# Performance work log

Measured on AMD Instinct MI355X. Metric: run time of the kernel, lower is better.

Reference implementation:

```python
import jax, jax.numpy as jnp
import numpy as np

TOP_P = 0.9
NEG_FILL = -100000.0
POS_FILL = 100000.0


def setup_inputs() -> dict:
    key = jax.random.key(0)
    k1, k2, k3 = jax.random.split(key, 3)
    B, S, V = 256, 128, 128000
    input_ids = jax.random.randint(k1, (B, S), 0, V, dtype=jnp.int64)
    logits = jax.random.normal(k2, (B, V), dtype=jnp.float32)
    # uniform watermark keys xi in (0,1); avoid exact 0 for log
    xi = jax.random.uniform(k3, (V,), dtype=jnp.float32, minval=1e-6, maxval=1.0)
    return {"input_ids": input_ids, "logits": logits, "xi": xi}


def reference(input_ids, logits, xi):
    B, V = logits.shape
    probs = jax.nn.softmax(logits, axis=-1)                       # [B, V]
    order = jnp.argsort(-probs, axis=-1)                          # descending sort indices [B, V]
    sorted_probs = jnp.take_along_axis(probs, order, axis=-1)     # [B, V]
    cum = jnp.cumsum(sorted_probs, axis=-1)                       # [B, V]
    # torch.searchsorted(cum, top_p, right=False) == count of cum < top_p
    cutoff = jnp.sum(cum < TOP_P, axis=-1)                        # [B]
    keep = jnp.arange(V)[None, :] <= cutoff[:, None]              # keep [:cutoff+1]
    # exponential-minimum trick: argmin over -log(xi)/p within the top-p set
    scores = -jnp.log(xi[order]) / sorted_probs                   # [B, V]
    scores = jnp.where(keep, scores, jnp.inf)
    pos = jnp.argmin(scores, axis=-1)                             # [B]
    next_token = jnp.take_along_axis(order, pos[:, None], axis=-1)[:, 0]  # [B]
    out = jnp.full_like(logits, NEG_FILL)
    out = out.at[jnp.arange(B), next_token].set(POS_FILL)
    return out
```

## Files before the change

kernel.cpp:

```cpp
#include <hip/hip_runtime.h>
#include <hip/hip_bf16.h>
#include <math.h>


constexpr int   NBINS     = 4096;
constexpr float BIN_MIN   = -8.0f;
constexpr float BIN_SCALE = 256.0f;
constexpr float BIN_OFF   = 2048.0f;
constexpr float BIN_W     = 1.0f / 256.0f;
constexpr int   STASH_CAP = 4096;
constexpr int   BINB_CAP  = 512;
constexpr int   WIN       = 6;
constexpr int   MAXC      = 96;
constexpr float CAND_THR  = -3.0f;
constexpr float NEG_FILL  = -100000.0f;
constexpr float POS_FILL  =  100000.0f;
constexpr float TOPP      = 0.9f;
constexpr int   BPR_FILL  = 32;

struct Ws {
    float*    key;
    unsigned* candIdx;
    float*    candKey;
    int*      candCnt;
    unsigned long long* winner;
};

__device__ __forceinline__ unsigned sortable(float f) {
    unsigned u = __float_as_uint(f);
    return (u & 0x80000000u) ? ~u : (u | 0x80000000u);
}
__device__ __forceinline__ int binOf(float l) {
    int b = (int)fmaf(l, BIN_SCALE, BIN_OFF);
    return min(max(b, 0), NBINS - 1);
}

__global__ __launch_bounds__(256)
void k0_keys(const float4* __restrict__ xi4, float* __restrict__ key,
             unsigned* __restrict__ candIdx, float* __restrict__ candKey,
             int* __restrict__ candCnt, int V4)
{
    __shared__ int cnt;
    __shared__ unsigned sIdx[MAXC];
    __shared__ float    sKey[MAXC];
    if (threadIdx.x == 0) cnt = 0;
    __syncthreads();

    const int f = blockIdx.x * 256 + threadIdx.x;
    if (f < V4) {
        float4 x = xi4[f];
        float kv[4];
        kv[0] = __logf(-__logf(x.x));
        kv[1] = __logf(-__logf(x.y));
        kv[2] = __logf(-__logf(x.z));
        kv[3] = __logf(-__logf(x.w));
        reinterpret_cast<float4*>(key)[f] = make_float4(kv[0], kv[1], kv[2], kv[3]);
        #pragma unroll
        for (int c = 0; c < 4; ++c) {
            if (kv[c] < CAND_THR) {
                int p = atomicAdd(&cnt, 1);
                if (p < MAXC) { sIdx[p] = (unsigned)(f * 4 + c); sKey[p] = kv[c]; }
            }
        }
    }
    __syncthreads();
    const int base = blockIdx.x * MAXC;
    const int n = min(cnt, MAXC);
    for (int i = threadIdx.x; i < MAXC; i += 256) {
        candIdx[base + i] = (i < n) ? sIdx[i] : 0u;
        candKey[base + i] = (i < n) ? sKey[i] : INFINITY;
    }
    if (threadIdx.x == 0) candCnt[blockIdx.x] = cnt;
}

__device__ __forceinline__ void scan_bins(const unsigned* lh, int lane,
                                          int& candBin, double& candS, double& target)
{
    const int hi = NBINS - 1 - (lane << 6);
    double seg = 0.0;
    for (int k = 0; k < 64; ++k) {
        int b = hi - k;
        seg += (double)lh[b] * (double)__expf(fmaf((float)b + 0.5f, BIN_W, BIN_MIN));
    }
    double v = seg;
    for (int off = 1; off < 64; off <<= 1) {
        double u = __shfl_up(v, off);
        if (lane >= off) v += u;
    }
    double excl = v - seg;
    double total = __shfl(v, 63);
    target = TOPP * total;

    candBin = -1; candS = 0.0;
    double cum = excl;
    for (int k = 0; k < 64; ++k) {
        int b = hi - k;
        double h = (double)lh[b] * (double)__expf(fmaf((float)b + 0.5f, BIN_W, BIN_MIN));
        if (candBin < 0 && cum + h >= target) { candBin = b; candS = cum; }
        cum += h;
    }
    for (int off = 32; off >= 1; off >>= 1) {
        int    ob = __shfl_xor(candBin, off);
        double os = __shfl_xor(candS, off);
        if (ob > candBin) { candBin = ob; candS = os; }
    }
}

__global__ __launch_bounds__(1024)
void kb_row(const float* __restrict__ logits, const float* __restrict__ key,
            const unsigned* __restrict__ candIdx, const float* __restrict__ candKey,
            const int* __restrict__ candCnt, unsigned long long* __restrict__ winner,
            int V, int nchunk, int nslots)
{
    const int row = blockIdx.x;
    const int tid = threadIdx.x;
    const int n4  = V >> 2;
    const float* rowp = logits + (size_t)row * V;
    const float4* p4 = reinterpret_cast<const float4*>(rowp);

    __shared__ unsigned lh[NBINS];
    __shared__ float  s_sl[STASH_CAP];
    __shared__ int    s_si[STASH_CAP];
    __shared__ float  s_bl[BINB_CAP];
    __shared__ int    s_bi[BINB_CAP];
    __shared__ double s_be[BINB_CAP];
    __shared__ unsigned long long wrd[16];
    __shared__ float  wrf[16];
    __shared__ int   sStashCnt, sB2, sBtil, sB, sM, sNeedFull, sCandOver;
    __shared__ float sLmax, sLcut;
    __shared__ int   sIcut;
    __shared__ double sCumAbove, sTarget;
    __shared__ unsigned long long sBest;

    for (int i = tid; i < NBINS; i += 1024) lh[i] = 0u;
    if (tid == 0) { sStashCnt = 0; sB2 = 0; sCandOver = 0; sNeedFull = 0; }
    __syncthreads();
    if (tid < nchunk && candCnt[tid] > MAXC) atomicOr(&sCandOver, 1);

    for (int k = 0; k < 8; ++k) {
        int j = tid + k * 4000;
        float4 L = p4[j];
        atomicAdd(&lh[binOf(L.x)], 1u);
        atomicAdd(&lh[binOf(L.y)], 1u);
        atomicAdd(&lh[binOf(L.z)], 1u);
        atomicAdd(&lh[binOf(L.w)], 1u);
    }
    __syncthreads();
    if (tid < 64) {
        int b; double cs, tg;
        scan_bins(lh, tid, b, cs, tg);
        if (tid == 0) sBtil = b;
    }
    __syncthreads();
    const int wlo = max(0, sBtil - WIN);
    const int whi = min(NBINS - 1, sBtil + WIN);

    for (int i = tid; i < NBINS; i += 1024) lh[i] = 0u;
    __syncthreads();

    float lmax = -INFINITY;
    for (int j = tid; j < n4; j += 1024) {
        float4 L = p4[j];
        float lv[4] = {L.x, L.y, L.z, L.w};
        #pragma unroll
        for (int c = 0; c < 4; ++c) {
            float l = lv[c];
            int b = binOf(l);
            atomicAdd(&lh[b], 1u);
            lmax = fmaxf(lmax, l);
            if ((unsigned)(b - wlo) <= (unsigned)(whi - wlo)) {
                int p = atomicAdd(&sStashCnt, 1);
                if (p < STASH_CAP) { s_sl[p] = l; s_si[p] = j * 4 + c; }
            }
        }
    }
    for (int off = 32; off >= 1; off >>= 1)
        lmax = fmaxf(lmax, __shfl_down(lmax, off));
    if ((tid & 63) == 0) wrf[tid >> 6] = lmax;
    __syncthreads();
    if (tid == 0) {
        float m = wrf[0];
        for (int w = 1; w < 16; ++w) m = fmaxf(m, wrf[w]);
        sLmax = m;
    }
    __syncthreads();

    if (tid < 64) {
        int b; double cs, tg;
        scan_bins(lh, tid, b, cs, tg);
        if (tid == 0) { sB = b; sCumAbove = cs; sTarget = tg; }
    }
    __syncthreads();
    const int B = sB;

    const bool stashOK = (B >= wlo) && (B <= whi) && (sStashCnt <= STASH_CAP);
    if (stashOK) {
        const int n = sStashCnt;
        for (int i = tid; i < n; i += 1024) {
            float l = s_sl[i];
            if (binOf(l) == B) {
                int q = atomicAdd(&sB2, 1);
                if (q < BINB_CAP) { s_bl[q] = l; s_bi[q] = s_si[i]; }
            }
        }
    } else {
        for (int j = tid; j < n4; j += 1024) {
            float4 L = p4[j];
            float lv[4] = {L.x, L.y, L.z, L.w};
            #pragma unroll
            for (int c = 0; c < 4; ++c) {
                if (binOf(lv[c]) == B) {
                    int q = atomicAdd(&sB2, 1);
                    if (q < BINB_CAP) { s_bl[q] = lv[c]; s_bi[q] = j * 4 + c; }
                }
            }
        }
    }
    __syncthreads();
    int nB = min(sB2, BINB_CAP);
    if (sB2 > BINB_CAP && tid == 0) sNeedFull = 1;

    int P = 1; while (P < nB) P <<= 1;
    if (P < 2) P = 2;
    for (int i = tid; i < P; i += 1024)
        if (i >= nB) { s_bl[i] = -INFINITY; s_bi[i] = 0x7fffffff; }
    for (int size = 2; size <= P; size <<= 1) {
        for (int stride = size >> 1; stride > 0; stride >>= 1) {
            __syncthreads();
            if (tid < P) {
                int i = tid, jj = tid ^ stride;
                if (jj > i) {
                    float li = s_bl[i], lj = s_bl[jj];
                    int   ii = s_bi[i], ij = s_bi[jj];
                    bool up = ((i & size) == 0);
                    bool iBeforeJ = (li > lj) || (li == lj && ii < ij);
                    bool sw = up ? (!iBeforeJ && !(li == lj && ii == ij)) : iBeforeJ;
                    if (sw) {
                        s_bl[i] = lj; s_bl[jj] = li;
                        s_bi[i] = ij; s_bi[jj] = ii;
                    }
                }
            }
        }
    }
    __syncthreads();

    for (int i = tid; i < nB; i += 1024) s_be[i] = exp((double)s_bl[i]);
    __syncthreads();
    if (tid == 0) {
        double cum = sCumAbove, target = sTarget;
        int m = nB;
        for (int k = 0; k < nB; ++k) {
            cum += s_be[k];
            if (cum >= target) { m = k + 1; break; }
        }
        m = max(m, 1);
        sM = m;
        sLcut = s_bl[m - 1];
        sIcut = s_bi[m - 1];
    }
    __syncthreads();
    const float lcut = sLcut;
    const int   icut = sIcut;

    unsigned long long best = ~0ull;
    for (int s = tid; s < nslots; s += 1024) {
        unsigned idx = candIdx[s];
        float ck = candKey[s];
        float l = rowp[idx];
        bool kept = (l > lcut) || (l == lcut && (int)idx <= icut);
        if (kept) {
            unsigned long long pack =
                ((unsigned long long)sortable(ck - l) << 32) | idx;
            best = pack < best ? pack : best;
        }
    }
    for (int off = 32; off >= 1; off >>= 1) {
        unsigned long long o = __shfl_down(best, off);
        best = o < best ? o : best;
    }
    if ((tid & 63) == 0) wrd[tid >> 6] = best;
    __syncthreads();
    if (tid == 0) {
        unsigned long long b = wrd[0];
        for (int w = 1; w < 16; ++w) b = wrd[w] < b ? wrd[w] : b;
        sBest = b;
        unsigned bound = sortable(CAND_THR - sLmax);
        if (!((unsigned)(b >> 32) < bound) || sCandOver) sNeedFull = 1;
    }
    __syncthreads();

    if (sNeedFull) {
        for (int j = tid; j < V; j += 1024) {
            float l = rowp[j];
            bool kept = (l > lcut) || (l == lcut && j <= icut);
            if (kept) {
                unsigned long long pack =
                    ((unsigned long long)sortable(key[j] - l) << 32) | (unsigned)j;
                best = pack < best ? pack : best;
            }
        }
        for (int off = 32; off >= 1; off >>= 1) {
            unsigned long long o = __shfl_down(best, off);
            best = o < best ? o : best;
        }
        if ((tid & 63) == 0) wrd[tid >> 6] = best;
        __syncthreads();
        if (tid == 0) {
            unsigned long long b = sBest;
            for (int w = 0; w < 16; ++w) b = wrd[w] < b ? wrd[w] : b;
            sBest = b;
        }
        __syncthreads();
    }

    if (tid == 0) winner[row] = sBest;
}

__global__ __launch_bounds__(256)
void kd_fill(float* __restrict__ out,
             const unsigned long long* __restrict__ winner, int V)
{
    const int row = blockIdx.x / BPR_FILL;
    const int seg = blockIdx.x % BPR_FILL;
    const int n4  = V >> 2;
    const int per = n4 / BPR_FILL;
    const int start = seg * per;
    const int end = (seg == BPR_FILL - 1) ? n4 : start + per;
    float4* o4 = reinterpret_cast<float4*>(out + (size_t)row * V);

    const unsigned win = (unsigned)(winner[row] & 0xffffffffu);
    const int winj = (int)(win >> 2);

    const float4 nf = make_float4(NEG_FILL, NEG_FILL, NEG_FILL, NEG_FILL);
    for (int j = start + threadIdx.x; j < end; j += 256) {
        float4 v = nf;
        if (j == winj) {
            float ov[4] = {v.x, v.y, v.z, v.w};
            ov[win & 3] = POS_FILL;
            v = make_float4(ov[0], ov[1], ov[2], ov[3]);
        }
        o4[j] = v;
    }
}

extern "C" void kernel_launch(void* const* d_in, const int* in_sizes, int n_in,
                              void* d_out, int out_size, void* d_ws, size_t ws_size,
                              hipStream_t stream) {
    const float* logits = (const float*)d_in[1];
    const float* xi     = (const float*)d_in[2];
    float*       out    = (float*)d_out;
    const int V = in_sizes[2];
    const int B = in_sizes[1] / V;
    const int V4 = V / 4;
    const int nchunk = (V + 1023) / 1024;
    const int nslots = nchunk * MAXC;

    char* w = (char*)d_ws;
    size_t off = 0;
    Ws ws;
    ws.key     = (float*)(w + off);    off += (size_t)V * sizeof(float);
    off = (off + 255) & ~(size_t)255;
    ws.candIdx = (unsigned*)(w + off); off += (size_t)nslots * sizeof(unsigned);
    ws.candKey = (float*)(w + off);    off += (size_t)nslots * sizeof(float);
    ws.candCnt = (int*)(w + off);      off += (size_t)nchunk * sizeof(int);
    off = (off + 255) & ~(size_t)255;
    ws.winner  = (unsigned long long*)(w + off); off += (size_t)B * sizeof(unsigned long long);

    k0_keys<<<(V4 + 255) / 256, 256, 0, stream>>>((const float4*)xi, ws.key,
                                                  ws.candIdx, ws.candKey, ws.candCnt, V4);
    kb_row <<<B, 1024, 0, stream>>>(logits, ws.key, ws.candIdx, ws.candKey,
                                    ws.candCnt, ws.winner, V, nchunk, nslots);
    kd_fill<<<B * BPR_FILL, 256, 0, stream>>>(out, ws.winner, V);
}
```

Before: 291.2 us.

## Split per-row histogram sweep across slice blocks and simplify bin resolution

The single per-row block that built the histogram and stash is split into a separate kernel where 8 blocks per row each histogram one slice and record a slice max, writing partial histograms to workspace. A resolve kernel sums the partials, rescans the full row for the boundary bin, and ranks bin members with an O(n^2) rank sort instead of a bitonic sort. This raises parallelism for the memory-bound sweep (256 blocks to 2048) but adds partial-histogram global traffic, an extra launch, and a second full row read in the resolve kernel since the stash is removed.

```diff
diff --git a/kernel.cpp b/kernel.cpp
--- a/kernel.cpp
+++ b/kernel.cpp
@@ -8,21 +8,22 @@
 constexpr float BIN_SCALE = 256.0f;
 constexpr float BIN_OFF   = 2048.0f;
 constexpr float BIN_W     = 1.0f / 256.0f;
-constexpr int   STASH_CAP = 4096;
 constexpr int   BINB_CAP  = 512;
-constexpr int   WIN       = 6;
 constexpr int   MAXC      = 96;
 constexpr float CAND_THR  = -3.0f;
 constexpr float NEG_FILL  = -100000.0f;
 constexpr float POS_FILL  =  100000.0f;
 constexpr float TOPP      = 0.9f;
 constexpr int   BPR_FILL  = 32;
+constexpr int   SLICES    = 8;
 
 struct Ws {
     float*    key;
     unsigned* candIdx;
     float*    candKey;
     int*      candCnt;
+    unsigned* phist;
+    float*    lmaxArr;
     unsigned long long* winner;
 };
 
@@ -73,6 +74,59 @@
     if (threadIdx.x == 0) candCnt[blockIdx.x] = cnt;
 }
 
+__global__ __launch_bounds__(256, 8)
+void k1_sweep(const float* __restrict__ logits, unsigned* __restrict__ phist,
+              float* __restrict__ lmaxArr, int V)
+{
+    const int row = blockIdx.x / SLICES;
+    const int sl  = blockIdx.x % SLICES;
+    const int n4  = V >> 2;
+    const int per = n4 / SLICES;
+    const float4* p4 = reinterpret_cast<const float4*>(logits + (size_t)row * V) + sl * per;
+
+    __shared__ unsigned lh[NBINS];
+    __shared__ float wrf[4];
+    for (int i = threadIdx.x; i < NBINS; i += 256) lh[i] = 0u;
+    __syncthreads();
+
+    float lmax = -INFINITY;
+    for (int base = 0; base < per; base += 1024) {
+        float4 r[4];
+        int    j[4];
+        #pragma unroll
+        for (int u = 0; u < 4; ++u) {
+            j[u] = base + u * 256 + threadIdx.x;
+            if (j[u] < per) r[u] = p4[j[u]];
+        }
+        #pragma unroll
+        for (int u = 0; u < 4; ++u) {
+            if (j[u] < per) {
+                float lv[4] = {r[u].x, r[u].y, r[u].z, r[u].w};
+                #pragma unroll
+                for (int c = 0; c < 4; ++c) {
+                    atomicAdd(&lh[binOf(lv[c])], 1u);
+                    lmax = fmaxf(lmax, lv[c]);
+                }
+            }
+        }
+    }
+    __syncthreads();
+
+    unsigned* dst = phist + ((size_t)row * SLICES + sl) * NBINS;
+    uint4* d4 = reinterpret_cast<uint4*>(dst);
+    const uint4* s4 = reinterpret_cast<const uint4*>(lh);
+    for (int i = threadIdx.x; i < NBINS / 4; i += 256) d4[i] = s4[i];
+
+    for (int off = 32; off >= 1; off >>= 1)
+        lmax = fmaxf(lmax, __shfl_down(lmax, off));
+    if ((threadIdx.x & 63) == 0) wrf[threadIdx.x >> 6] = lmax;
+    __syncthreads();
+    if (threadIdx.x == 0) {
+        float m = fmaxf(fmaxf(wrf[0], wrf[1]), fmaxf(wrf[2], wrf[3]));
+        lmaxArr[row * SLICES + sl] = m;
+    }
+}
+
 __device__ __forceinline__ void scan_bins(const unsigned* lh, int lane,
                                           int& candBin, double& candS, double& target)
 {
@@ -107,10 +161,12 @@
 }
 
 __global__ __launch_bounds__(1024)
-void kb_row(const float* __restrict__ logits, const float* __restrict__ key,
-            const unsigned* __restrict__ candIdx, const float* __restrict__ candKey,
-            const int* __restrict__ candCnt, unsigned long long* __restrict__ winner,
-            int V, int nchunk, int nslots)
+void k2_resolve(const float* __restrict__ logits, const float* __restrict__ key,
+                const unsigned* __restrict__ phist, const float* __restrict__ lmaxArr,
+                const unsigned* __restrict__ candIdx, const float* __restrict__ candKey,
+                const int* __restrict__ candCnt,
+                unsigned long long* __restrict__ winner,
+                int V, int nchunk, int nslots)
 {
     const int row = blockIdx.x;
     const int tid = threadIdx.x;
@@ -119,71 +175,28 @@
     const float4* p4 = reinterpret_cast<const float4*>(rowp);
 
     __shared__ unsigned lh[NBINS];
-    __shared__ float  s_sl[STASH_CAP];
-    __shared__ int    s_si[STASH_CAP];
     __shared__ float  s_bl[BINB_CAP];
     __shared__ int    s_bi[BINB_CAP];
+    __shared__ float  s_sl[BINB_CAP];
+    __shared__ int    s_si[BINB_CAP];
     __shared__ double s_be[BINB_CAP];
     __shared__ unsigned long long wrd[16];
-    __shared__ float  wrf[16];
-    __shared__ int   sStashCnt, sB2, sBtil, sB, sM, sNeedFull, sCandOver;
-    __shared__ float sLmax, sLcut;
+    __shared__ int   sB2, sB, sNeedFull;
+    __shared__ float sLcut;
     __shared__ int   sIcut;
     __shared__ double sCumAbove, sTarget;
     __shared__ unsigned long long sBest;
 
-    for (int i = tid; i < NBINS; i += 1024) lh[i] = 0u;
-    if (tid == 0) { sStashCnt = 0; sB2 = 0; sCandOver = 0; sNeedFull = 0; }
-    __syncthreads();
-    if (tid < nchunk && candCnt[tid] > MAXC) atomicOr(&sCandOver, 1);
-
-    for (int k = 0; k < 8; ++k) {
-        int j = tid + k * 4000;
-        float4 L = p4[j];
-        atomicAdd(&lh[binOf(L.x)], 1u);
-        atomicAdd(&lh[binOf(L.y)], 1u);
-        atomicAdd(&lh[binOf(L.z)], 1u);
-        atomicAdd(&lh[binOf(L.w)], 1u);
-    }
-    __syncthreads();
-    if (tid < 64) {
-        int b; double cs, tg;
-        scan_bins(lh, tid, b, cs, tg);
-        if (tid == 0) sBtil = b;
-    }
-    __syncthreads();
-    const int wlo = max(0, sBtil - WIN);
-    const int whi = min(NBINS - 1, sBtil + WIN);
-
-    for (int i = tid; i < NBINS; i += 1024) lh[i] = 0u;
-    __syncthreads();
-
-    float lmax = -INFINITY;
-    for (int j = tid; j < n4; j += 1024) {
-        float4 L = p4[j];
-        float lv[4] = {L.x, L.y, L.z, L.w};
-        #pragma unroll
-        for (int c = 0; c < 4; ++c) {
-            float l = lv[c];
-            int b = binOf(l);
-            atomicAdd(&lh[b], 1u);
-            lmax = fmaxf(lmax, l);
-            if ((unsigned)(b - wlo) <= (unsigned)(whi - wlo)) {
-                int p = atomicAdd(&sStashCnt, 1);
-                if (p < STASH_CAP) { s_sl[p] = l; s_si[p] = j * 4 + c; }
-            }
-        }
-    }
-    for (int off = 32; off >= 1; off >>= 1)
-        lmax = fmaxf(lmax, __shfl_down(lmax, off));
-    if ((tid & 63) == 0) wrf[tid >> 6] = lmax;
-    __syncthreads();
-    if (tid == 0) {
-        float m = wrf[0];
-        for (int w = 1; w < 16; ++w) m = fmaxf(m, wrf[w]);
-        sLmax = m;
-    }
-    __syncthreads();
+    const unsigned* ph = phist + (size_t)row * SLICES * NBINS;
+    for (int i = tid; i < NBINS; i += 1024) {
+        unsigned s = 0;
+        #pragma unroll
+        for (int k = 0; k < SLICES; ++k) s += ph[k * NBINS + i];
+        lh[i] = s;
+    }
+    if (tid == 0) { sB2 = 0; sNeedFull = 0; }
+    __syncthreads();
+    if (tid < nchunk && candCnt[tid] > MAXC) atomicOr(&sNeedFull, 1);
 
     if (tid < 64) {
         int b; double cs, tg;
@@ -193,59 +206,43 @@
     __syncthreads();
     const int B = sB;
 
-    const bool stashOK = (B >= wlo) && (B <= whi) && (sStashCnt <= STASH_CAP);
-    if (stashOK) {
-        const int n = sStashCnt;
-        for (int i = tid; i < n; i += 1024) {
-            float l = s_sl[i];
-            if (binOf(l) == B) {
-                int q = atomicAdd(&sB2, 1);
-                if (q < BINB_CAP) { s_bl[q] = l; s_bi[q] = s_si[i]; }
-            }
-        }
-    } else {
-        for (int j = tid; j < n4; j += 1024) {
-            float4 L = p4[j];
-            float lv[4] = {L.x, L.y, L.z, L.w};
-            #pragma unroll
-            for (int c = 0; c < 4; ++c) {
-                if (binOf(lv[c]) == B) {
-                    int q = atomicAdd(&sB2, 1);
-                    if (q < BINB_CAP) { s_bl[q] = lv[c]; s_bi[q] = j * 4 + c; }
-                }
-            }
-        }
-    }
-    __syncthreads();
-    int nB = min(sB2, BINB_CAP);
-    if (sB2 > BINB_CAP && tid == 0) sNeedFull = 1;
-
-    int P = 1; while (P < nB) P <<= 1;
-    if (P < 2) P = 2;
-    for (int i = tid; i < P; i += 1024)
-        if (i >= nB) { s_bl[i] = -INFINITY; s_bi[i] = 0x7fffffff; }
-    for (int size = 2; size <= P; size <<= 1) {
-        for (int stride = size >> 1; stride > 0; stride >>= 1) {
-            __syncthreads();
-            if (tid < P) {
-                int i = tid, jj = tid ^ stride;
-                if (jj > i) {
-                    float li = s_bl[i], lj = s_bl[jj];
-                    int   ii = s_bi[i], ij = s_bi[jj];
-                    bool up = ((i & size) == 0);
-                    bool iBeforeJ = (li > lj) || (li == lj && ii < ij);
-                    bool sw = up ? (!iBeforeJ && !(li == lj && ii == ij)) : iBeforeJ;
-                    if (sw) {
-                        s_bl[i] = lj; s_bl[jj] = li;
-                        s_bi[i] = ij; s_bi[jj] = ii;
+    for (int base = 0; base < n4; base += 4096) {
+        float4 r[4];
+        int    j[4];
+        #pragma unroll
+        for (int u = 0; u < 4; ++u) {
+            j[u] = base + u * 1024 + tid;
+            if (j[u] < n4) r[u] = p4[j[u]];
+        }
+        #pragma unroll
+        for (int u = 0; u < 4; ++u) {
+            if (j[u] < n4) {
+                float lv[4] = {r[u].x, r[u].y, r[u].z, r[u].w};
+                #pragma unroll
+                for (int c = 0; c < 4; ++c) {
+                    if (binOf(lv[c]) == B) {
+                        int q = atomicAdd(&sB2, 1);
+                        if (q < BINB_CAP) { s_bl[q] = lv[c]; s_bi[q] = j[u] * 4 + c; }
                     }
                 }
             }
         }
     }
     __syncthreads();
-
-    for (int i = tid; i < nB; i += 1024) s_be[i] = exp((double)s_bl[i]);
+    const int nB = min(sB2, BINB_CAP);
+
+    for (int i = tid; i < nB; i += 1024) {
+        float li = s_bl[i]; int ii = s_bi[i];
+        int r = 0;
+        for (int j = 0; j < nB; ++j) {
+            float lj = s_bl[j]; int ij = s_bi[j];
+            r += (lj > li) || (lj == li && ij < ii);
+        }
+        s_sl[r] = li; s_si[r] = ii;
+    }
+    __syncthreads();
+
+    for (int i = tid; i < nB; i += 1024) s_be[i] = exp((double)s_sl[i]);
     __syncthreads();
     if (tid == 0) {
         double cum = sCumAbove, target = sTarget;
@@ -255,9 +252,8 @@
             if (cum >= target) { m = k + 1; break; }
         }
         m = max(m, 1);
-        sM = m;
-        sLcut = s_bl[m - 1];
-        sIcut = s_bi[m - 1];
+        if (nB == 0) { sNeedFull = 1; sLcut = (float)B * BIN_W + BIN_MIN; sIcut = 0x7fffffff; }
+        else { sLcut = s_sl[m - 1]; sIcut = s_si[m - 1]; }
     }
     __syncthreads();
     const float lcut = sLcut;
@@ -285,8 +281,10 @@
         unsigned long long b = wrd[0];
         for (int w = 1; w < 16; ++w) b = wrd[w] < b ? wrd[w] : b;
         sBest = b;
-        unsigned bound = sortable(CAND_THR - sLmax);
-        if (!((unsigned)(b >> 32) < bound) || sCandOver) sNeedFull = 1;
+        float lmax = -INFINITY;
+        for (int k = 0; k < SLICES; ++k) lmax = fmaxf(lmax, lmaxArr[row * SLICES + k]);
+        unsigned bound = sortable(CAND_THR - lmax);
+        if (!((unsigned)(b >> 32) < bound)) sNeedFull = 1;
     }
     __syncthreads();
 
@@ -365,11 +363,16 @@
     ws.candKey = (float*)(w + off);    off += (size_t)nslots * sizeof(float);
     ws.candCnt = (int*)(w + off);      off += (size_t)nchunk * sizeof(int);
     off = (off + 255) & ~(size_t)255;
+    ws.phist   = (unsigned*)(w + off); off += (size_t)B * SLICES * NBINS * sizeof(unsigned);
+    ws.lmaxArr = (float*)(w + off);    off += (size_t)B * SLICES * sizeof(float);
+    off = (off + 255) & ~(size_t)255;
     ws.winner  = (unsigned long long*)(w + off); off += (size_t)B * sizeof(unsigned long long);
 
-    k0_keys<<<(V4 + 255) / 256, 256, 0, stream>>>((const float4*)xi, ws.key,
-                                                  ws.candIdx, ws.candKey, ws.candCnt, V4);
-    kb_row <<<B, 1024, 0, stream>>>(logits, ws.key, ws.candIdx, ws.candKey,
-                                    ws.candCnt, ws.winner, V, nchunk, nslots);
-    kd_fill<<<B * BPR_FILL, 256, 0, stream>>>(out, ws.winner, V);
-}
+    k0_keys   <<<(V4 + 255) / 256, 256, 0, stream>>>((const float4*)xi, ws.key,
+                                                     ws.candIdx, ws.candKey, ws.candCnt, V4);
+    k1_sweep  <<<B * SLICES, 256, 0, stream>>>(logits, ws.phist, ws.lmaxArr, V);
+    k2_resolve<<<B, 1024, 0, stream>>>(logits, ws.key, ws.phist, ws.lmaxArr,
+                                       ws.candIdx, ws.candKey, ws.candCnt,
+                                       ws.winner, V, nchunk, nslots);
+    kd_fill   <<<B * BPR_FILL, 256, 0, stream>>>(out, ws.winner, V);
+}
```

New measurement: 320.4 us. +10.1%, slower.
